# Performance work log

Hardware: AMD Instinct MI355X
Metric: run time of the kernel (lower is better)

The kernel has to match this reference:

```python
import jax, jax.numpy as jnp
import numpy as np

B, S, D, C = 2, 4096, 768, 8192
SCALE = 1.0
LN_EPS = 1e-5


def setup_inputs() -> dict:
    key = jax.random.key(0)
    ks = jax.random.split(key, 8)
    std = 0.03
    return {
        "x": jax.random.normal(ks[0], (B, S, D), dtype=jnp.float32),
        "attention_masks": jax.random.randint(ks[1], (B, S), 0, 2).astype(jnp.int32),
        "Wk": jax.random.normal(ks[2], (D, D), dtype=jnp.float32) * std,
        "Wv": jax.random.normal(ks[3], (D, D), dtype=jnp.float32) * std,
        "bv": jnp.zeros((D,), dtype=jnp.float32),
        "Q": jax.random.normal(ks[4], (C, D), dtype=jnp.float32) * std,  # label_representations
        "ln_gamma": jnp.ones((D,), dtype=jnp.float32),
        "ln_beta": jnp.zeros((D,), dtype=jnp.float32),
        "w_out": jax.random.normal(ks[5], (D,), dtype=jnp.float32) * std,  # output_linear.weight [1, D]
        "b_out": jnp.zeros((), dtype=jnp.float32),  # output_linear.bias [1]
    }


def reference(x, attention_masks, Wk, Wv, bv, Q, ln_gamma, ln_beta, w_out, b_out):
    # K, V projections (torch Linear: x @ W.T + b)
    K = jnp.einsum("bsd,ed->bse", x, Wk)
    V = jnp.einsum("bsd,ed->bse", x, Wv) + bv
    # label-query cross-attention scores: [B, C, S]
    scores = jnp.einsum("cd,bsd->bcs", Q, K)
    # additive mask: -inf where attention_masks == 0 (intended semantics of pad/repeat/masked_fill)
    scores = jnp.where(attention_masks[:, None, :] == 0, -jnp.inf, scores)
    attn = jax.nn.softmax(scores / SCALE, axis=2)  # [B, C, S]
    y = jnp.einsum("bcs,bsd->bcd", attn, V)  # [B, C, D]
    # LayerNorm over last dim
    mu = jnp.mean(y, axis=-1, keepdims=True)
    var = jnp.mean((y - mu) ** 2, axis=-1, keepdims=True)
    y = (y - mu) * jax.lax.rsqrt(var + LN_EPS) * ln_gamma + ln_beta
    # elementwise weight-mul-sum output head: [B, C]
    return jnp.einsum("bcd,d->bc", y, w_out) + b_out
```

## Files before the change

kernel.cpp:

```cpp
#include <hip/hip_runtime.h>
#include <hip/hip_bf16.h>
#include <hip/hip_fp16.h>

typedef _Float16 f16x8 __attribute__((ext_vector_type(8)));
typedef _Float16 f16x4 __attribute__((ext_vector_type(4)));
typedef float f32x4 __attribute__((ext_vector_type(4)));

#define AS1 __attribute__((address_space(1)))
#define AS3 __attribute__((address_space(3)))
#define MFMA16(a, b, c) __builtin_amdgcn_mfma_f32_16x16x32_f16(a, b, c, 0, 0, 0)
#define BARRIER asm volatile("s_barrier" ::: "memory")

#define LDP 2304

__global__ __launch_bounds__(256) void maskscan(const int* __restrict__ am,
                                                int* __restrict__ idx,
                                                int* __restrict__ meta) {
  const int b = blockIdx.x, t = threadIdx.x;
  const int* m = am + (size_t)b * 4096;
  int* ix = idx + (size_t)b * 4096;
  __shared__ int cnt[256];
  __shared__ int pre[257];
  int loc[16], c = 0;
#pragma unroll
  for (int j = 0; j < 16; ++j) {
    loc[j] = m[t * 16 + j];
    c += (loc[j] != 0);
  }
  cnt[t] = c;
  __syncthreads();
  if (t == 0) {
    pre[0] = 0;
    for (int i = 0; i < 256; ++i) pre[i + 1] = pre[i] + cnt[i];
  }
  __syncthreads();
  int p = pre[t];
#pragma unroll
  for (int j = 0; j < 16; ++j)
    if (loc[j]) ix[p++] = t * 16 + j;
  const int valid = pre[256];
  int nsp = ((valid + 255) >> 8) << 8;
  if (nsp < 512) nsp = 512;
  for (int j = valid + t; j < nsp; j += 256) ix[j] = -1;
  if (t == 0) { meta[2 * b] = valid; meta[2 * b + 1] = nsp; }
}

__global__ __launch_bounds__(192) void gather_cvt(const float* __restrict__ x,
                                                  const int* __restrict__ idx,
                                                  const int* __restrict__ meta,
                                                  unsigned short* __restrict__ xc) {
  const int b = blockIdx.y, row = blockIdx.x, t = threadIdx.x;
  if (row >= meta[2 * b + 1]) return;
  const int src = idx[(size_t)b * 4096 + row];
  unsigned short* dst = xc + ((size_t)b * 4096 + row) * 768 + t * 4;
  f16x4 h;
  if (src < 0) {
    h[0] = h[1] = h[2] = h[3] = (_Float16)0.0f;
  } else {
    float4 v = *(const float4*)(x + ((size_t)b * 4096 + src) * 768 + t * 4);
    h[0] = (_Float16)v.x; h[1] = (_Float16)v.y; h[2] = (_Float16)v.z; h[3] = (_Float16)v.w;
  }
  *(f16x4*)dst = h;
}

__global__ __launch_bounds__(256) void cvt_f32_f16(const float* __restrict__ in,
                                                   unsigned short* __restrict__ out,
                                                   int n8) {
  int i = blockIdx.x * 256 + threadIdx.x;
  if (i >= n8) return;
  const float4* p = (const float4*)in + 2 * (size_t)i;
  float4 a = p[0], b = p[1];
  f16x8 h;
  h[0] = (_Float16)a.x; h[1] = (_Float16)a.y; h[2] = (_Float16)a.z; h[3] = (_Float16)a.w;
  h[4] = (_Float16)b.x; h[5] = (_Float16)b.y; h[6] = (_Float16)b.z; h[7] = (_Float16)b.w;
  *(f16x8*)(out + (size_t)i * 8) = h;
}

template <int OMODE, bool RBIAS, int EXITD>
__global__ __launch_bounds__(256) void gemm_nt(const unsigned short* __restrict__ A, int lda,
                                               const unsigned short* __restrict__ B, int ldb,
                                               void* __restrict__ Cout, int ldc,
                                               const float* __restrict__ bias,
                                               const int* __restrict__ meta,
                                               int N, int K) {
  const int nbn = N >> 7;
  const int bm = blockIdx.x / nbn, bn = blockIdx.x % nbn;
  if constexpr (EXITD == 1) {
    if (((bm & 31) << 7) >= meta[2 * (bm >> 5) + 1]) return;
  } else if constexpr (EXITD == 2) {
    if (((bn & 31) << 7) >= meta[2 * (bn >> 5) + 1]) return;
  }
  __shared__ __attribute__((aligned(16))) unsigned short As[128 * 64];
  __shared__ __attribute__((aligned(16))) unsigned short Bs[128 * 64];
  const int tid = threadIdx.x;
  const int w = tid >> 6, l = tid & 63;
  const int wr = w >> 1, wc = w & 1;
  const int lr = l & 15, lg = l >> 4;

  const unsigned short* Ab = A + (size_t)bm * 128 * lda;
  const unsigned short* Bb = B + (size_t)bn * 128 * ldb;

  f32x4 acc[4][4] = {};

  auto ldfrag = [&](const unsigned short* base, int row, int kk) {
    int off = row * 128 + kk * 64 + lg * 16;
    off ^= (row & 7) << 4;
    return *(const f16x8*)((const unsigned char*)base + off);
  };

  for (int kt = 0; kt < K; kt += 64) {
#pragma unroll
    for (int i = 0; i < 4; ++i) {
      const int c = i * 256 + w * 64 + l;
      const int row = c >> 3, col = (((c & 7) ^ (row & 7)) << 3);
      __builtin_amdgcn_global_load_lds((const AS1 void*)(Ab + (size_t)row * lda + kt + col),
                                       (AS3 void*)(As + (i * 256 + w * 64) * 8), 16, 0, 0);
    }
#pragma unroll
    for (int i = 0; i < 4; ++i) {
      const int c = i * 256 + w * 64 + l;
      const int row = c >> 3, col = (((c & 7) ^ (row & 7)) << 3);
      __builtin_amdgcn_global_load_lds((const AS1 void*)(Bb + (size_t)row * ldb + kt + col),
                                       (AS3 void*)(Bs + (i * 256 + w * 64) * 8), 16, 0, 0);
    }
    __syncthreads();
#pragma unroll
    for (int kk = 0; kk < 2; ++kk) {
      f16x8 af[4], bf[4];
#pragma unroll
      for (int mi = 0; mi < 4; ++mi) af[mi] = ldfrag(As, wr * 64 + mi * 16 + lr, kk);
#pragma unroll
      for (int ni = 0; ni < 4; ++ni) bf[ni] = ldfrag(Bs, wc * 64 + ni * 16 + lr, kk);
#pragma unroll
      for (int mi = 0; mi < 4; ++mi)
#pragma unroll
        for (int ni = 0; ni < 4; ++ni)
          acc[mi][ni] = MFMA16(af[mi], bf[ni], acc[mi][ni]);
    }
    __syncthreads();
  }

#pragma unroll
  for (int mi = 0; mi < 4; ++mi) {
#pragma unroll
    for (int r = 0; r < 4; ++r) {
      const int row = bm * 128 + wr * 64 + mi * 16 + lg * 4 + r;
      const float badd = RBIAS ? bias[row] : 0.0f;
#pragma unroll
      for (int ni = 0; ni < 4; ++ni) {
        const int col = bn * 128 + wc * 64 + ni * 16 + lr;
        float v = acc[mi][ni][r] + badd;
        if constexpr (OMODE == 0)
          ((unsigned short*)Cout)[(size_t)row * ldc + col] =
              __builtin_bit_cast(unsigned short, (_Float16)v);
        else
          ((float*)Cout)[(size_t)row * ldc + col] = v;
      }
    }
  }
}

template <int EPI>
__global__ __launch_bounds__(512, 2) void gemm256(
    const unsigned short* __restrict__ A, int lda, size_t sAz,
    const unsigned short* __restrict__ B, int ldb, size_t sBz,
    unsigned short* __restrict__ Cout, int ldc, size_t sCz, size_t sCk,
    const int* __restrict__ meta, int NTfix) {
  __shared__ __attribute__((aligned(16))) unsigned char lds[131072];
  const int tid = threadIdx.x;
  const int wv = tid >> 6, l = tid & 63;
  const int wm = wv >> 2, wn = wv & 3;
  const int lr = l & 15, lg = l >> 4;
  const int bid = blockIdx.x;

  const int xr = ((lr >> 1) & 3) << 4;
  const int aoff = ((wm * 128 + lr) << 6) + ((lg << 4) ^ xr);
  const int boff = ((wn * 64 + lr) << 6) + ((lg << 4) ^ xr);

  const unsigned short* Ab = nullptr;
  const unsigned short* Bb = nullptr;

  auto stage = [&](int uu) {
    const int tau = uu >> 2, r = uu & 3;
    const int regionOff = ((tau & 1) << 16) | ((r & 1) << 15) | ((r >> 1) << 14);
    const unsigned short* base = (r & 1) ? Bb : Ab;
    const int ld = (r & 1) ? ldb : lda;
    const int kcol0 = tau * 64 + ((r >> 1) << 5);
#pragma unroll
    for (int j = 0; j < 2; ++j) {
      const int row = wv * 32 + j * 16 + (l >> 2);
      const int col = kcol0 + ((((l & 3) ^ ((row >> 1) & 3))) << 3);
      __builtin_amdgcn_global_load_lds(
          (const AS1 void*)(base + (size_t)row * ld + col),
          (AS3 void*)(lds + regionOff + wv * 2048 + j * 1024), 16, 0, 0);
    }
  };

  constexpr int NPASS = (EPI == 2) ? 2 : 1;

  for (int pass = 0; pass < NPASS; ++pass) {
    int z, bm, bn, NT, koff, ks = 0;
    if constexpr (EPI == 2) {
      if (pass == 0) {
        z = bid >> 8;
        const int rem = bid & 255;
        bm = rem & 31;
        bn = rem >> 5;
        if (bn * 256 >= meta[2 * z + 1]) continue;
      } else {
        const int tn0 = max(0, (meta[1] >> 8) - 8);
        const int tn1 = max(0, (meta[3] >> 8) - 8);
        if (bid >= 32 * (tn0 + tn1)) break;
        int t = bid;
        if (t < 32 * tn0) { z = 0; }
        else { t -= 32 * tn0; z = 1; }
        bm = t & 31;
        bn = 8 + (t >> 5);
      }
      NT = NTfix;
      koff = 0;
    } else {
      z = bid / 192;
      const int r = bid - z * 192;
      ks = r / 96;
      const int q = r - ks * 96;
      bm = q & 31;
      bn = q >> 5;
      const int nsp = meta[2 * z + 1];
      NT = nsp >> 7;
      koff = ks * (nsp >> 1);
    }
    const int valid = meta[2 * z];

    Ab = A + (size_t)z * sAz + koff + (size_t)bm * 256 * lda;
    Bb = B + (size_t)z * sBz + koff + (size_t)bn * 256 * ldb;

    const int NT4 = NT * 4;
    f32x4 acc[8][4] = {};
    f16x8 Ac[4], An[4], Bc[4], B2[4];

    auto rdA4 = [&](f16x8* d, int mh, int kk, int bo) {
#pragma unroll
      for (int i = 0; i < 4; ++i)
        d[i] = *(const f16x8*)(lds + bo + (kk << 14) + aoff + (4 * mh + i) * 1024);
    };
    auto rdB4 = [&](f16x8* d, int kk, int bo) {
#pragma unroll
      for (int i = 0; i < 4; ++i)
        d[i] = *(const f16x8*)(lds + 32768 + bo + (kk << 14) + boff + i * 1024);
    };
    auto mm16 = [&](const f16x8* Aq, const f16x8* Bq, int mh) {
#pragma unroll
      for (int i = 0; i < 4; ++i)
#pragma unroll
        for (int j = 0; j < 4; ++j)
          acc[4 * mh + i][j] = MFMA16(Aq[i], Bq[j], acc[4 * mh + i][j]);
    };

    for (int i = 0; i < 6; ++i) stage(i);
    int u = 6;
    asm volatile("s_waitcnt vmcnt(4)" ::: "memory");
    BARRIER;

    for (int t = 0; t < NT; ++t) {
      const int bo = (t & 1) << 16;
      rdB4(Bc, 0, bo);
      rdA4(Ac, 0, 0, bo);
      if (u < NT4) stage(u);
      ++u;
      __builtin_amdgcn_s_setprio(1);
      rdA4(An, 1, 0, bo);
      mm16(Ac, Bc, 0);
      __builtin_amdgcn_s_setprio(0);
      BARRIER;
      if (u < NT4) stage(u);
      ++u;
      __builtin_amdgcn_s_setprio(1);
      rdB4(B2, 1, bo);
      rdA4(Ac, 0, 1, bo);
      mm16(An, Bc, 1);
      __builtin_amdgcn_s_setprio(0);
      BARRIER;
      if (u < NT4) stage(u);
      ++u;
      __builtin_amdgcn_s_setprio(1);
      rdA4(An, 1, 1, bo);
      mm16(Ac, B2, 0);
      __builtin_amdgcn_s_setprio(0);
      BARRIER;
      if (u < NT4) stage(u);
      ++u;
      __builtin_amdgcn_s_setprio(1);
      mm16(An, B2, 1);
      __builtin_amdgcn_s_setprio(0);
      if (t + 2 < NT) {
        asm volatile("s_waitcnt vmcnt(4)" ::: "memory");
      } else if (t + 2 == NT) {
        asm volatile("s_waitcnt vmcnt(0)" ::: "memory");
      }
      BARRIER;
    }

    const size_t crow0 = (size_t)bm * 256 + wm * 128;
    const int ccol0 = bn * 256 + wn * 64;
    unsigned short* Cz = Cout + (size_t)z * sCz + (size_t)ks * sCk;
#pragma unroll
    for (int mf = 0; mf < 8; ++mf) {
#pragma unroll
      for (int rr = 0; rr < 4; ++rr) {
        const size_t rb = (crow0 + mf * 16 + lg * 4 + rr) * (size_t)ldc;
#pragma unroll
        for (int nf = 0; nf < 4; ++nf) {
          const int col = ccol0 + nf * 16 + lr;
          float v = acc[mf][nf][rr];
          if constexpr (EPI == 2) v = (col < valid) ? __expf(v) : 0.0f;
          Cz[rb + col] = __builtin_bit_cast(unsigned short, (_Float16)v);
        }
      }
    }
  }
}

__device__ inline float block_sum(float v, float* sh, int t) {
#pragma unroll
  for (int o = 32; o; o >>= 1) v += __shfl_xor(v, o);
  __syncthreads();
  if ((t & 63) == 0) sh[t >> 6] = v;
  __syncthreads();
  return sh[0] + sh[1] + sh[2] + sh[3];
}

__global__ __launch_bounds__(256) void ln_head(const unsigned short* __restrict__ yp,
                                               size_t zoff, size_t koff,
                                               const float* __restrict__ gam,
                                               const float* __restrict__ bet,
                                               const float* __restrict__ wo,
                                               const float* __restrict__ bo,
                                               float* __restrict__ out) {
  const int z = blockIdx.y;
  const size_t rbase = (size_t)z * zoff + (size_t)blockIdx.x * 768;
  const _Float16* y0 = (const _Float16*)yp + rbase;
  const _Float16* y1 = y0 + koff;
  const int t = threadIdx.x;
  float a0 = (float)y0[t] + (float)y1[t];
  float a1 = (float)y0[t + 256] + (float)y1[t + 256];
  float a2 = (float)y0[t + 512] + (float)y1[t + 512];
  __shared__ float sh[4];
  float s = block_sum(a0 + a1 + a2, sh, t);
  float mu = s * (1.0f / 768.0f);
  float d0 = a0 - mu, d1 = a1 - mu, d2 = a2 - mu;
  float q = block_sum(d0 * d0 + d1 * d1 + d2 * d2, sh, t);
  float rs = rsqrtf(q * (1.0f / 768.0f) + 1e-5f);
  float o = (d0 * rs * gam[t] + bet[t]) * wo[t] +
            (d1 * rs * gam[t + 256] + bet[t + 256]) * wo[t + 256] +
            (d2 * rs * gam[t + 512] + bet[t + 512]) * wo[t + 512];
  o = block_sum(o, sh, t);
  if (t == 0) out[(size_t)z * 8192 + blockIdx.x] = o + bo[0];
}

extern "C" void kernel_launch(void* const* d_in, const int* in_sizes, int n_in,
                              void* d_out, int out_size, void* d_ws, size_t ws_size,
                              hipStream_t stream) {
  const float* x  = (const float*)d_in[0];
  const int*   am = (const int*)d_in[1];
  const float* Wk = (const float*)d_in[2];
  const float* Wv = (const float*)d_in[3];
  const float* bv = (const float*)d_in[4];
  const float* Q  = (const float*)d_in[5];
  const float* gam = (const float*)d_in[6];
  const float* bet = (const float*)d_in[7];
  const float* wo  = (const float*)d_in[8];
  const float* bo  = (const float*)d_in[9];
  float* out = (float*)d_out;

  const int S = 4096, D = 768, C = 8192;
  const size_t nX = (size_t)2 * S * D;
  const size_t nW = (size_t)D * D;
  const size_t nQ = (size_t)C * D;
  const size_t nPc = (size_t)C * LDP;
  const size_t nY = (size_t)C * D;

  unsigned short* xc  = (unsigned short*)d_ws;
  unsigned short* Wkb = xc + nX;
  unsigned short* Wvb = Wkb + nW;
  unsigned short* Qb  = Wvb + nW;
  unsigned short* Kb  = Qb + nQ;
  unsigned short* Vt  = Kb + nX;
  unsigned short* P   = Vt + nX;
  unsigned short* yp  = P + 2 * nPc;
  int* idx  = (int*)(yp + 4 * nY);
  int* meta = idx + 2 * 4096;

  maskscan<<<2, 256, 0, stream>>>(am, idx, meta);
  gather_cvt<<<dim3(4096, 2), 192, 0, stream>>>(x, idx, meta, xc);

  cvt_f32_f16<<<(int)(nW / 8 / 256), 256, 0, stream>>>(Wk, Wkb, (int)(nW / 8));
  cvt_f32_f16<<<(int)(nW / 8 / 256), 256, 0, stream>>>(Wv, Wvb, (int)(nW / 8));
  cvt_f32_f16<<<(int)(nQ / 8 / 256), 256, 0, stream>>>(Q, Qb, (int)(nQ / 8));

  gemm_nt<0, false, 1><<<(8192 / 128) * (768 / 128), 256, 0, stream>>>(
      xc, D, Wkb, D, Kb, D, nullptr, meta, 768, D);
  gemm_nt<0, true, 2><<<(768 / 128) * (8192 / 128), 256, 0, stream>>>(
      Wvb, D, xc, D, Vt, 2 * S, bv, meta, 2 * S, D);

  gemm256<2><<<dim3(512, 1), 512, 0, stream>>>(
      Qb, D, 0, Kb, D, (size_t)S * D, P, LDP, nPc, 0, meta, 12);

  gemm256<0><<<dim3(384, 1), 512, 0, stream>>>(
      P, LDP, nPc, Vt, 2 * S, (size_t)S, yp, D, 2 * nY, nY, meta, 0);

  ln_head<<<dim3(C, 2), 256, 0, stream>>>(yp, 2 * nY, nY, gam, bet, wo, bo, out);
}
```

Baseline: 224.7 us.

## Prefetch next tile's first LDS fragments during last MFMA phase of gemm256

Restructures the gemm256 main loop so the first A/B register fragments for the next K-tile are read from the other LDS buffer during the final MFMA group of the current tile, instead of at the start of each iteration. The vmcnt wait is moved earlier, before the last barrier, and tightened to vmcnt(2) so the next buffer is ready when it is read. Launch bounds are relaxed from 2 to 1 block per CU, giving the compiler more registers for the extra live fragments at the cost of occupancy. Some buffer variables are renamed.

```diff
diff --git a/kernel.cpp b/kernel.cpp
--- a/kernel.cpp
+++ b/kernel.cpp
@@ -161,7 +161,7 @@
 }
 
 template <int EPI>
-__global__ __launch_bounds__(512, 2) void gemm256(
+__global__ __launch_bounds__(512, 1) void gemm256(
     const unsigned short* __restrict__ A, int lda, size_t sAz,
     const unsigned short* __restrict__ B, int ldb, size_t sBz,
     unsigned short* __restrict__ Cout, int ldc, size_t sCz, size_t sCk,
@@ -177,13 +177,13 @@
   const int aoff = ((wm * 128 + lr) << 6) + ((lg << 4) ^ xr);
   const int boff = ((wn * 64 + lr) << 6) + ((lg << 4) ^ xr);
 
-  const unsigned short* Ab = nullptr;
-  const unsigned short* Bb = nullptr;
+  const unsigned short* Abase = nullptr;
+  const unsigned short* Bbase = nullptr;
 
   auto stage = [&](int uu) {
     const int tau = uu >> 2, r = uu & 3;
     const int regionOff = ((tau & 1) << 16) | ((r & 1) << 15) | ((r >> 1) << 14);
-    const unsigned short* base = (r & 1) ? Bb : Ab;
+    const unsigned short* base = (r & 1) ? Bbase : Abase;
     const int ld = (r & 1) ? ldb : lda;
     const int kcol0 = tau * 64 + ((r >> 1) << 5);
 #pragma unroll
@@ -232,12 +232,12 @@
     }
     const int valid = meta[2 * z];
 
-    Ab = A + (size_t)z * sAz + koff + (size_t)bm * 256 * lda;
-    Bb = B + (size_t)z * sBz + koff + (size_t)bn * 256 * ldb;
+    Abase = A + (size_t)z * sAz + koff + (size_t)bm * 256 * lda;
+    Bbase = B + (size_t)z * sBz + koff + (size_t)bn * 256 * ldb;
 
     const int NT4 = NT * 4;
     f32x4 acc[8][4] = {};
-    f16x8 Ac[4], An[4], Bc[4], B2[4];
+    f16x8 Ar0[4], Ar1[4], Br0[4], Br1[4];
 
     auto rdA4 = [&](f16x8* d, int mh, int kk, int bo) {
 #pragma unroll
@@ -261,43 +261,48 @@
     int u = 6;
     asm volatile("s_waitcnt vmcnt(4)" ::: "memory");
     BARRIER;
+    rdA4(Ar0, 0, 0, 0);
+    rdB4(Br0, 0, 0);
 
     for (int t = 0; t < NT; ++t) {
       const int bo = (t & 1) << 16;
-      rdB4(Bc, 0, bo);
-      rdA4(Ac, 0, 0, bo);
+      const int bo2 = bo ^ 65536;
       if (u < NT4) stage(u);
       ++u;
       __builtin_amdgcn_s_setprio(1);
-      rdA4(An, 1, 0, bo);
-      mm16(Ac, Bc, 0);
+      rdA4(Ar1, 1, 0, bo);
+      mm16(Ar0, Br0, 0);
       __builtin_amdgcn_s_setprio(0);
       BARRIER;
       if (u < NT4) stage(u);
       ++u;
       __builtin_amdgcn_s_setprio(1);
-      rdB4(B2, 1, bo);
-      rdA4(Ac, 0, 1, bo);
-      mm16(An, Bc, 1);
+      rdA4(Ar0, 0, 1, bo);
+      rdB4(Br1, 1, bo);
+      mm16(Ar1, Br0, 1);
       __builtin_amdgcn_s_setprio(0);
       BARRIER;
       if (u < NT4) stage(u);
       ++u;
       __builtin_amdgcn_s_setprio(1);
-      rdA4(An, 1, 1, bo);
-      mm16(Ac, B2, 0);
+      rdA4(Ar1, 1, 1, bo);
+      mm16(Ar0, Br1, 0);
       __builtin_amdgcn_s_setprio(0);
+      if (t + 2 < NT) {
+        asm volatile("s_waitcnt vmcnt(2)" ::: "memory");
+      } else if (t + 2 == NT) {
+        asm volatile("s_waitcnt vmcnt(0)" ::: "memory");
+      }
       BARRIER;
       if (u < NT4) stage(u);
       ++u;
       __builtin_amdgcn_s_setprio(1);
-      mm16(An, B2, 1);
+      if (t + 1 < NT) {
+        rdA4(Ar0, 0, 0, bo2);
+        rdB4(Br0, 0, bo2);
+      }
+      mm16(Ar1, Br1, 1);
       __builtin_amdgcn_s_setprio(0);
-      if (t + 2 < NT) {
-        asm volatile("s_waitcnt vmcnt(4)" ::: "memory");
-      } else if (t + 2 == NT) {
-        asm volatile("s_waitcnt vmcnt(0)" ::: "memory");
-      }
       BARRIER;
     }
 
```

New measurement: 224.7 us. Within noise of the previous version (+0.0%).

## Split PV GEMM K into four slices with XCD-aware tile mapping

Applied to the files above, without the earlier changes.

Raises the split-K factor of the P·V GEMM from 2 to 4, which doubles the grid to 768 blocks, and widens the partial-output buffer so ln_head sums four partials. Block IDs are remapped so neighbouring tiles of the same batch land on the same XCD (bid&7), aiming for better L2 reuse in both GEMM256 passes. Launch bounds drop to 1 block per CU, so the compiler may use more registers. The cost is more partial-sum traffic and a longer reduction in ln_head.

```diff
diff --git a/kernel.cpp b/kernel.cpp
--- a/kernel.cpp
+++ b/kernel.cpp
@@ -161,7 +161,7 @@
 }
 
 template <int EPI>
-__global__ __launch_bounds__(512, 2) void gemm256(
+__global__ __launch_bounds__(512, 1) void gemm256(
     const unsigned short* __restrict__ A, int lda, size_t sAz,
     const unsigned short* __restrict__ B, int ldb, size_t sBz,
     unsigned short* __restrict__ Cout, int ldc, size_t sCz, size_t sCk,
@@ -177,13 +177,13 @@
   const int aoff = ((wm * 128 + lr) << 6) + ((lg << 4) ^ xr);
   const int boff = ((wn * 64 + lr) << 6) + ((lg << 4) ^ xr);
 
-  const unsigned short* Ab = nullptr;
-  const unsigned short* Bb = nullptr;
+  const unsigned short* Abase = nullptr;
+  const unsigned short* Bbase = nullptr;
 
   auto stage = [&](int uu) {
     const int tau = uu >> 2, r = uu & 3;
     const int regionOff = ((tau & 1) << 16) | ((r & 1) << 15) | ((r >> 1) << 14);
-    const unsigned short* base = (r & 1) ? Bb : Ab;
+    const unsigned short* base = (r & 1) ? Bbase : Abase;
     const int ld = (r & 1) ? ldb : lda;
     const int kcol0 = tau * 64 + ((r >> 1) << 5);
 #pragma unroll
@@ -202,10 +202,11 @@
     int z, bm, bn, NT, koff, ks = 0;
     if constexpr (EPI == 2) {
       if (pass == 0) {
-        z = bid >> 8;
-        const int rem = bid & 255;
-        bm = rem & 31;
-        bn = rem >> 5;
+        const int xcd = bid & 7, s = bid >> 3;
+        z = xcd >> 2;
+        const int q = xcd & 3;
+        bm = ((q & 1) << 4) + (s & 7) + ((s >> 5) << 3);
+        bn = ((q >> 1) << 2) + ((s >> 3) & 3);
         if (bn * 256 >= meta[2 * z + 1]) continue;
       } else {
         const int tn0 = max(0, (meta[1] >> 8) - 8);
@@ -220,20 +221,19 @@
       NT = NTfix;
       koff = 0;
     } else {
-      z = bid / 192;
-      const int r = bid - z * 192;
-      ks = r / 96;
-      const int q = r - ks * 96;
-      bm = q & 31;
-      bn = q >> 5;
+      const int xcd = bid & 7, s = bid >> 3;
+      z = xcd >> 2;
+      ks = xcd & 3;
+      bm = s / 3;
+      bn = s - 3 * bm;
       const int nsp = meta[2 * z + 1];
-      NT = nsp >> 7;
-      koff = ks * (nsp >> 1);
+      NT = nsp >> 8;
+      koff = ks * (nsp >> 2);
     }
     const int valid = meta[2 * z];
 
-    Ab = A + (size_t)z * sAz + koff + (size_t)bm * 256 * lda;
-    Bb = B + (size_t)z * sBz + koff + (size_t)bn * 256 * ldb;
+    Abase = A + (size_t)z * sAz + koff + (size_t)bm * 256 * lda;
+    Bbase = B + (size_t)z * sBz + koff + (size_t)bn * 256 * ldb;
 
     const int NT4 = NT * 4;
     f32x4 acc[8][4] = {};
@@ -341,10 +341,12 @@
   const size_t rbase = (size_t)z * zoff + (size_t)blockIdx.x * 768;
   const _Float16* y0 = (const _Float16*)yp + rbase;
   const _Float16* y1 = y0 + koff;
+  const _Float16* y2 = y1 + koff;
+  const _Float16* y3 = y2 + koff;
   const int t = threadIdx.x;
-  float a0 = (float)y0[t] + (float)y1[t];
-  float a1 = (float)y0[t + 256] + (float)y1[t + 256];
-  float a2 = (float)y0[t + 512] + (float)y1[t + 512];
+  float a0 = (float)y0[t] + (float)y1[t] + (float)y2[t] + (float)y3[t];
+  float a1 = (float)y0[t + 256] + (float)y1[t + 256] + (float)y2[t + 256] + (float)y3[t + 256];
+  float a2 = (float)y0[t + 512] + (float)y1[t + 512] + (float)y2[t + 512] + (float)y3[t + 512];
   __shared__ float sh[4];
   float s = block_sum(a0 + a1 + a2, sh, t);
   float mu = s * (1.0f / 768.0f);
@@ -388,7 +390,7 @@
   unsigned short* Vt  = Kb + nX;
   unsigned short* P   = Vt + nX;
   unsigned short* yp  = P + 2 * nPc;
-  int* idx  = (int*)(yp + 4 * nY);
+  int* idx  = (int*)(yp + 8 * nY);
   int* meta = idx + 2 * 4096;
 
   maskscan<<<2, 256, 0, stream>>>(am, idx, meta);
@@ -406,8 +408,8 @@
   gemm256<2><<<dim3(512, 1), 512, 0, stream>>>(
       Qb, D, 0, Kb, D, (size_t)S * D, P, LDP, nPc, 0, meta, 12);
 
-  gemm256<0><<<dim3(384, 1), 512, 0, stream>>>(
-      P, LDP, nPc, Vt, 2 * S, (size_t)S, yp, D, 2 * nY, nY, meta, 0);
-
-  ln_head<<<dim3(C, 2), 256, 0, stream>>>(yp, 2 * nY, nY, gam, bet, wo, bo, out);
-}
+  gemm256<0><<<dim3(768, 1), 512, 0, stream>>>(
+      P, LDP, nPc, Vt, 2 * S, (size_t)S, yp, D, 4 * nY, nY, meta, 0);
+
+  ln_head<<<dim3(C, 2), 256, 0, stream>>>(yp, 4 * nY, nY, gam, bet, wo, bo, out);
+}
```

After: 232.4 us. 1.03x slower.

## Split PV GEMM into three K slices and fuse weight conversions

Applied to the files above, without the earlier changes.

The attention-times-V GEMM now splits the reduction dimension three ways instead of two, raising the grid from 384 to 576 blocks. Slice lengths are computed in 64-wide units so uneven valid lengths still partition correctly. The LayerNorm head sums three partial outputs, and the workspace grows to hold them. The three f32-to-f16 weight conversion launches are merged into one kernel, and gemm256's launch bounds drop the two-blocks-per-CU hint, which may change register allocation. The extra split-K partials cost more memory traffic in exchange for better CU occupancy.

```diff
diff --git a/kernel.cpp b/kernel.cpp
--- a/kernel.cpp
+++ b/kernel.cpp
@@ -63,17 +63,27 @@
   *(f16x4*)dst = h;
 }
 
-__global__ __launch_bounds__(256) void cvt_f32_f16(const float* __restrict__ in,
-                                                   unsigned short* __restrict__ out,
-                                                   int n8) {
-  int i = blockIdx.x * 256 + threadIdx.x;
-  if (i >= n8) return;
-  const float4* p = (const float4*)in + 2 * (size_t)i;
+__global__ __launch_bounds__(256) void cvt3(const float* __restrict__ wk,
+                                            const float* __restrict__ wv,
+                                            const float* __restrict__ q,
+                                            unsigned short* __restrict__ wkb,
+                                            unsigned short* __restrict__ wvb,
+                                            unsigned short* __restrict__ qb,
+                                            int nW8, int nQ8) {
+  const int i = blockIdx.x * 256 + threadIdx.x;
+  const float* in;
+  unsigned short* out;
+  int r;
+  if (i < nW8) { in = wk; out = wkb; r = i; }
+  else if (i < 2 * nW8) { in = wv; out = wvb; r = i - nW8; }
+  else if (i < 2 * nW8 + nQ8) { in = q; out = qb; r = i - 2 * nW8; }
+  else return;
+  const float4* p = (const float4*)in + 2 * (size_t)r;
   float4 a = p[0], b = p[1];
   f16x8 h;
   h[0] = (_Float16)a.x; h[1] = (_Float16)a.y; h[2] = (_Float16)a.z; h[3] = (_Float16)a.w;
   h[4] = (_Float16)b.x; h[5] = (_Float16)b.y; h[6] = (_Float16)b.z; h[7] = (_Float16)b.w;
-  *(f16x8*)(out + (size_t)i * 8) = h;
+  *(f16x8*)(out + (size_t)r * 8) = h;
 }
 
 template <int OMODE, bool RBIAS, int EXITD>
@@ -161,7 +171,7 @@
 }
 
 template <int EPI>
-__global__ __launch_bounds__(512, 2) void gemm256(
+__global__ __launch_bounds__(512, 1) void gemm256(
     const unsigned short* __restrict__ A, int lda, size_t sAz,
     const unsigned short* __restrict__ B, int ldb, size_t sBz,
     unsigned short* __restrict__ Cout, int ldc, size_t sCz, size_t sCk,
@@ -177,13 +187,13 @@
   const int aoff = ((wm * 128 + lr) << 6) + ((lg << 4) ^ xr);
   const int boff = ((wn * 64 + lr) << 6) + ((lg << 4) ^ xr);
 
-  const unsigned short* Ab = nullptr;
-  const unsigned short* Bb = nullptr;
+  const unsigned short* Abase = nullptr;
+  const unsigned short* Bbase = nullptr;
 
   auto stage = [&](int uu) {
     const int tau = uu >> 2, r = uu & 3;
     const int regionOff = ((tau & 1) << 16) | ((r & 1) << 15) | ((r >> 1) << 14);
-    const unsigned short* base = (r & 1) ? Bb : Ab;
+    const unsigned short* base = (r & 1) ? Bbase : Abase;
     const int ld = (r & 1) ? ldb : lda;
     const int kcol0 = tau * 64 + ((r >> 1) << 5);
 #pragma unroll
@@ -220,20 +230,22 @@
       NT = NTfix;
       koff = 0;
     } else {
-      z = bid / 192;
-      const int r = bid - z * 192;
+      z = bid / 288;
+      const int r = bid - z * 288;
       ks = r / 96;
       const int q = r - ks * 96;
       bm = q & 31;
       bn = q >> 5;
       const int nsp = meta[2 * z + 1];
-      NT = nsp >> 7;
-      koff = ks * (nsp >> 1);
+      const int uk = nsp >> 6;
+      const int u0 = (uk + 2) / 3;
+      koff = ks * u0 * 64;
+      NT = (ks < 2) ? u0 : (uk - 2 * u0);
     }
     const int valid = meta[2 * z];
 
-    Ab = A + (size_t)z * sAz + koff + (size_t)bm * 256 * lda;
-    Bb = B + (size_t)z * sBz + koff + (size_t)bn * 256 * ldb;
+    Abase = A + (size_t)z * sAz + koff + (size_t)bm * 256 * lda;
+    Bbase = B + (size_t)z * sBz + koff + (size_t)bn * 256 * ldb;
 
     const int NT4 = NT * 4;
     f32x4 acc[8][4] = {};
@@ -341,10 +353,11 @@
   const size_t rbase = (size_t)z * zoff + (size_t)blockIdx.x * 768;
   const _Float16* y0 = (const _Float16*)yp + rbase;
   const _Float16* y1 = y0 + koff;
+  const _Float16* y2 = y1 + koff;
   const int t = threadIdx.x;
-  float a0 = (float)y0[t] + (float)y1[t];
-  float a1 = (float)y0[t + 256] + (float)y1[t + 256];
-  float a2 = (float)y0[t + 512] + (float)y1[t + 512];
+  float a0 = (float)y0[t] + (float)y1[t] + (float)y2[t];
+  float a1 = (float)y0[t + 256] + (float)y1[t + 256] + (float)y2[t + 256];
+  float a2 = (float)y0[t + 512] + (float)y1[t + 512] + (float)y2[t + 512];
   __shared__ float sh[4];
   float s = block_sum(a0 + a1 + a2, sh, t);
   float mu = s * (1.0f / 768.0f);
@@ -388,15 +401,17 @@
   unsigned short* Vt  = Kb + nX;
   unsigned short* P   = Vt + nX;
   unsigned short* yp  = P + 2 * nPc;
-  int* idx  = (int*)(yp + 4 * nY);
+  int* idx  = (int*)(yp + 6 * nY);
   int* meta = idx + 2 * 4096;
 
   maskscan<<<2, 256, 0, stream>>>(am, idx, meta);
   gather_cvt<<<dim3(4096, 2), 192, 0, stream>>>(x, idx, meta, xc);
 
-  cvt_f32_f16<<<(int)(nW / 8 / 256), 256, 0, stream>>>(Wk, Wkb, (int)(nW / 8));
-  cvt_f32_f16<<<(int)(nW / 8 / 256), 256, 0, stream>>>(Wv, Wvb, (int)(nW / 8));
-  cvt_f32_f16<<<(int)(nQ / 8 / 256), 256, 0, stream>>>(Q, Qb, (int)(nQ / 8));
+  {
+    const int nW8 = (int)(nW / 8), nQ8 = (int)(nQ / 8);
+    const int tot = 2 * nW8 + nQ8;
+    cvt3<<<(tot + 255) / 256, 256, 0, stream>>>(Wk, Wv, Q, Wkb, Wvb, Qb, nW8, nQ8);
+  }
 
   gemm_nt<0, false, 1><<<(8192 / 128) * (768 / 128), 256, 0, stream>>>(
       xc, D, Wkb, D, Kb, D, nullptr, meta, 768, D);
@@ -406,8 +421,8 @@
   gemm256<2><<<dim3(512, 1), 512, 0, stream>>>(
       Qb, D, 0, Kb, D, (size_t)S * D, P, LDP, nPc, 0, meta, 12);
 
-  gemm256<0><<<dim3(384, 1), 512, 0, stream>>>(
-      P, LDP, nPc, Vt, 2 * S, (size_t)S, yp, D, 2 * nY, nY, meta, 0);
-
-  ln_head<<<dim3(C, 2), 256, 0, stream>>>(yp, 2 * nY, nY, gam, bet, wo, bo, out);
-}
+  gemm256<0><<<dim3(576, 1), 512, 0, stream>>>(
+      P, LDP, nPc, Vt, 2 * S, (size_t)S, yp, D, 3 * nY, nY, meta, 0);
+
+  ln_head<<<dim3(C, 2), 256, 0, stream>>>(yp, 3 * nY, nY, gam, bet, wo, bo, out);
+}
```

Result: slower. 236.4 us (+5.2%).
